# Kernel tuning notes

Measured on AMD Instinct MI355X. Metric: run time of the kernel, lower is better.

## Reference

```python
import jax, jax.numpy as jnp
import numpy as np

D_MODEL = 1024
N_HEADS = 16
HEAD_DIM = D_MODEL // N_HEADS
Q_PROJ = D_MODEL // 2
KV_PROJ = D_MODEL
INIT_SCALE = 0.02
EPS = 1e-5


def _ln(x, g, b):
    mu = jnp.mean(x, axis=-1, keepdims=True)
    var = jnp.mean(jnp.square(x - mu), axis=-1, keepdims=True)
    return (x - mu) * jax.lax.rsqrt(var + EPS) * g + b


def setup_inputs() -> dict:
    key = jax.random.key(0)
    ks = jax.random.split(key, 8)
    B, S = 2, 2048
    x = jax.random.normal(ks[0], (B, S, D_MODEL), dtype=jnp.float32)
    W_dq = INIT_SCALE * jax.random.normal(ks[1], (D_MODEL, Q_PROJ), dtype=jnp.float32)
    W_uq = INIT_SCALE * jax.random.normal(ks[2], (Q_PROJ, D_MODEL), dtype=jnp.float32)
    W_dkv = INIT_SCALE * jax.random.normal(ks[3], (D_MODEL, KV_PROJ), dtype=jnp.float32)
    W_ukv = INIT_SCALE * jax.random.normal(ks[4], (KV_PROJ, 2 * D_MODEL), dtype=jnp.float32)
    wo = INIT_SCALE * jax.random.normal(ks[5], (D_MODEL, D_MODEL), dtype=jnp.float32)
    return {
        "x": x,
        "W_dq": W_dq, "W_uq": W_uq,
        "q_ln_g": jnp.ones((Q_PROJ,), jnp.float32), "q_ln_b": jnp.zeros((Q_PROJ,), jnp.float32),
        "W_dkv": W_dkv, "W_ukv": W_ukv,
        "kv_ln_g": jnp.ones((KV_PROJ,), jnp.float32), "kv_ln_b": jnp.zeros((KV_PROJ,), jnp.float32),
        "preq_g": jnp.ones((D_MODEL,), jnp.float32), "preq_b": jnp.zeros((D_MODEL,), jnp.float32),
        "prekv_g": jnp.ones((D_MODEL,), jnp.float32), "prekv_b": jnp.zeros((D_MODEL,), jnp.float32),
        "wo": wo,
    }


def reference(x, W_dq, W_uq, q_ln_g, q_ln_b, W_dkv, W_ukv, kv_ln_g, kv_ln_b,
              preq_g, preq_b, prekv_g, prekv_b, wo):
    B, S, D = x.shape
    H, dh = N_HEADS, HEAD_DIM
    # Q path: pre-norm -> low-rank down -> LN -> up
    x_q = _ln(x, preq_g, preq_b)
    cq = _ln(x_q @ W_dq, q_ln_g, q_ln_b)            # [B,S,D/2]
    Q = (cq @ W_uq).reshape(B, S, H, dh)             # [B,S,H,dh]
    Q = Q / jnp.sqrt(jnp.asarray(dh, x.dtype))
    # KV path: pre-norm -> compress -> LN -> up, split into K,V
    x_kv = _ln(x, prekv_g, prekv_b)
    ckv = _ln(x_kv @ W_dkv, kv_ln_g, kv_ln_b)        # [B,S,D]
    KV = ckv @ W_ukv                                 # [B,S,2D]
    K, V = jnp.split(KV, 2, axis=-1)
    K = K.reshape(B, S, H, dh)
    V = V.reshape(B, S, H, dh)
    # causal attention (scores materialized as in original)
    scores = jnp.einsum('bqhd,bkhd->bhqk', Q, K)     # [B,H,S,S]
    causal = jnp.tril(jnp.ones((S, S), dtype=bool))  # True where allowed
    scores = jnp.where(causal[None, None], scores, jnp.asarray(-jnp.inf, scores.dtype))
    attn = jax.nn.softmax(scores, axis=-1)
    out = jnp.einsum('bhqk,bkhd->bqhd', attn, V).reshape(B, S, D)
    return out @ wo.T
```

## Files before the change

### kernel.cpp

```cpp
#include <hip/hip_runtime.h>
#include <hip/hip_bf16.h>

#define SEQ   2048
#define BATCH 2
#define NROWS 4096
#define DM    1024
#define NHEAD 16
#define DH    64
#define QP    512
#define KVP   1024
#define CH    4

typedef unsigned short us;
typedef ushort4 us4;
using bf16x8 = __attribute__((ext_vector_type(8))) __bf16;
using f32x4  = __attribute__((ext_vector_type(4))) float;

__device__ __forceinline__ us f2bf(float f) {
  union { __hip_bfloat16 h; us u; } cv;
  cv.h = __float2bfloat16(f);
  return cv.u;
}
__device__ __forceinline__ float bf2f(us u) {
  union { unsigned int u32; float f; } cv;
  cv.u32 = ((unsigned int)u) << 16;
  return cv.f;
}
__device__ __forceinline__ float loadp(const void* p, long i, int isbf) {
  return isbf ? bf2f(((const us*)p)[i]) : ((const float*)p)[i];
}
__device__ __forceinline__ void async16(const void* g, void* l) {
  __builtin_amdgcn_global_load_lds((__attribute__((address_space(1))) void*)g,
                                   (__attribute__((address_space(3))) void*)l,
                                   16, 0, 0);
}
__device__ __forceinline__ unsigned cvtpk(float lo, float hi) {
  unsigned r;
  asm("v_cvt_pk_bf16_f32 %0, %1, %2" : "=v"(r) : "v"(lo), "v"(hi));
  return r;
}

__global__ void detect_dtype(const us* __restrict__ xu, int* __restrict__ flag) {
  __shared__ int red[256];
  const int tid = threadIdx.x;
  int cnt = 0;
  for (int i = tid; i < 4096; i += 256) {
    const int e = (xu[i] >> 7) & 0xff;
    if (e == 0 || (e >= 100 && e <= 134)) cnt++;
  }
  red[tid] = cnt;
  __syncthreads();
  for (int s = 128; s; s >>= 1) {
    if (tid < s) red[tid] += red[tid + s];
    __syncthreads();
  }
  if (tid == 0) *flag = (red[0] >= 3900) ? 1 : 0;
}

struct TD { const void* in; us* out; int R, C, nt, trans; };

__global__ __launch_bounds__(256) void stage0(
    TD t0, TD t1, TD t2, TD t3, TD t4,
    float4* __restrict__ zp, int n4,
    const void* __restrict__ xin,
    const void* __restrict__ g1, const void* __restrict__ b1,
    const void* __restrict__ g2, const void* __restrict__ b2,
    us* __restrict__ out1, us* __restrict__ out2,
    const int* __restrict__ flag)
{
  __shared__ us tile[32][33];
  __shared__ float red[8];
  __shared__ float musd[2];
  const int tid = threadIdx.x;
  const int isbf = *flag;
  int lin = blockIdx.x;

  if (lin < 5120) {
    TD t = t0;
    if (lin >= t.nt) { lin -= t.nt; t = t1;
      if (lin >= t.nt) { lin -= t.nt; t = t2;
        if (lin >= t.nt) { lin -= t.nt; t = t3;
          if (lin >= t.nt) { lin -= t.nt; t = t4; } } } }
    const int ntx = t.C >> 5;
    const int by = lin / ntx, bx = lin - by * ntx;
    const int tx = tid & 31, ty = tid >> 5;
    const long r0 = (long)by * 32, c0 = (long)bx * 32;
    if (t.trans) {
#pragma unroll
      for (int i = 0; i < 32; i += 8)
        tile[ty + i][tx] = isbf ? ((const us*)t.in)[(r0 + ty + i) * t.C + c0 + tx]
                                : f2bf(((const float*)t.in)[(r0 + ty + i) * t.C + c0 + tx]);
      __syncthreads();
#pragma unroll
      for (int i = 0; i < 32; i += 8)
        t.out[(c0 + ty + i) * t.R + r0 + tx] = tile[tx][ty + i];
    } else {
#pragma unroll
      for (int i = 0; i < 32; i += 8)
        t.out[(r0 + ty + i) * t.C + c0 + tx] =
            isbf ? ((const us*)t.in)[(r0 + ty + i) * t.C + c0 + tx]
                 : f2bf(((const float*)t.in)[(r0 + ty + i) * t.C + c0 + tx]);
    }
    return;
  }
  if (lin < 6144) {
    const float4 z = {0.f, 0.f, 0.f, 0.f};
    for (int i = (lin - 5120) * 256 + tid; i < n4; i += 1024 * 256) zp[i] = z;
    return;
  }
  const long row = lin - 6144;
  float v[4];
  float s = 0.f, s2 = 0.f;
#pragma unroll
  for (int i = 0; i < 4; i++) {
    const long c = tid + i * 256;
    const float t = loadp(xin, row * 1024 + c, isbf);
    v[i] = t; s += t; s2 += t * t;
  }
#pragma unroll
  for (int off = 32; off > 0; off >>= 1) {
    s  += __shfl_down(s,  off);
    s2 += __shfl_down(s2, off);
  }
  const int wave = tid >> 6, lane = tid & 63;
  if (lane == 0) { red[wave] = s; red[4 + wave] = s2; }
  __syncthreads();
  if (tid == 0) {
    const float ts = red[0] + red[1] + red[2] + red[3];
    const float t2 = red[4] + red[5] + red[6] + red[7];
    const float mu = ts * (1.f / 1024.f);
    const float var = t2 * (1.f / 1024.f) - mu * mu;
    musd[0] = mu; musd[1] = rsqrtf(var + 1e-5f);
  }
  __syncthreads();
  const float mu = musd[0], rs = musd[1];
#pragma unroll
  for (int i = 0; i < 4; i++) {
    const long c = tid + i * 256;
    const float nrm = (v[i] - mu) * rs;
    out1[row * 1024 + c] = f2bf(nrm * loadp(g1, c, isbf) + loadp(b1, c, isbf));
    out2[row * 1024 + c] = f2bf(nrm * loadp(g2, c, isbf) + loadp(b2, c, isbf));
  }
}

template<int C>
__device__ __forceinline__ void ln_body(const us* __restrict__ in,
                                        const void* __restrict__ g, const void* __restrict__ b,
                                        us* __restrict__ out, long row, int tid, int isbf) {
  constexpr int NP = C / 256;
  float v[NP];
  float s = 0.f, s2 = 0.f;
#pragma unroll
  for (int i = 0; i < NP; i++) {
    const float t = bf2f(in[row * C + tid + i * 256]);
    v[i] = t; s += t; s2 += t * t;
  }
#pragma unroll
  for (int off = 32; off > 0; off >>= 1) {
    s  += __shfl_down(s,  off);
    s2 += __shfl_down(s2, off);
  }
  __shared__ float red[8];
  __shared__ float musd[2];
  const int wave = tid >> 6, lane = tid & 63;
  if (lane == 0) { red[wave] = s; red[4 + wave] = s2; }
  __syncthreads();
  if (tid == 0) {
    const float ts = red[0] + red[1] + red[2] + red[3];
    const float t2 = red[4] + red[5] + red[6] + red[7];
    const float mu = ts * (1.f / C);
    const float var = t2 * (1.f / C) - mu * mu;
    musd[0] = mu; musd[1] = rsqrtf(var + 1e-5f);
  }
  __syncthreads();
  const float mu = musd[0], rs = musd[1];
#pragma unroll
  for (int i = 0; i < NP; i++) {
    const long c = tid + i * 256;
    out[row * C + c] = f2bf((v[i] - mu) * rs * loadp(g, c, isbf) + loadp(b, c, isbf));
  }
}

__global__ __launch_bounds__(256) void ln_rows_pair(
    const us* __restrict__ inq, const void* __restrict__ qg, const void* __restrict__ qb,
    us* __restrict__ outq,
    const us* __restrict__ inkv, const void* __restrict__ kvg, const void* __restrict__ kvb,
    us* __restrict__ outkv,
    const int* __restrict__ flag)
{
  const int isbf = *flag;
  if (blockIdx.x < NROWS)
    ln_body<512>(inq, qg, qb, outq, blockIdx.x, threadIdx.x, isbf);
  else
    ln_body<1024>(inkv, kvg, kvb, outkv, blockIdx.x - NROWS, threadIdx.x, isbf);
}

struct GD { const us* A; const us* Bt; void* C; int N, K, nxs; float scale; int omode; };

__global__ __launch_bounds__(256) void gemm_mt(GD g0, GD g1, int nb0,
                                               const int* __restrict__ flag) {
  __shared__ us As[2][128 * 32];
  __shared__ us Bs[2][128 * 32];
  GD g;
  int lin = blockIdx.x;
  {
    const int cpx = gridDim.x >> 3;
    lin = (lin & 7) * cpx + (lin >> 3);
  }
  if (lin < nb0) g = g0; else { g = g1; lin -= nb0; }
  const int by = lin >> g.nxs;
  const int bx = lin - (by << g.nxs);
  const int N = g.N, K = g.K;

  const int tid  = threadIdx.x;
  const int lane = tid & 63;
  const int wave = tid >> 6;
  const int n16  = lane & 15;
  const int quad = lane >> 4;
  const long m0 = (long)by * 128;
  const long n0 = (long)bx * 128;
  const int wm = (wave >> 1) * 64;
  const int wn = (wave & 1) * 64;

  const f32x4 zero = {0.f, 0.f, 0.f, 0.f};
  f32x4 acc[4][4];
#pragma unroll
  for (int i = 0; i < 4; i++)
#pragma unroll
    for (int j = 0; j < 4; j++) acc[i][j] = zero;

  const int srow = tid >> 2;
  const int scol = (tid & 3) * 8;
  const us* Ag0 = g.A  + (m0 + srow) * K + scol;
  const us* Ag1 = g.A  + (m0 + 64 + srow) * K + scol;
  const us* Bg0 = g.Bt + (n0 + srow) * K + scol;
  const us* Bg1 = g.Bt + (n0 + 64 + srow) * K + scol;
  const int lds_off = srow * 32 + scol;

  for (int k0 = 0; k0 < K; k0 += 64) {
#pragma unroll
    for (int s = 0; s < 2; s++) {
      const int ks = k0 + s * 32;
      async16(Ag0 + ks, As[s] + lds_off);
      async16(Ag1 + ks, As[s] + 2048 + lds_off);
      async16(Bg0 + ks, Bs[s] + lds_off);
      async16(Bg1 + ks, Bs[s] + 2048 + lds_off);
    }
    __syncthreads();
#pragma unroll
    for (int s = 0; s < 2; s++) {
      bf16x8 af[4], bfv[4];
#pragma unroll
      for (int i = 0; i < 4; i++)
        af[i] = *(const bf16x8*)(As[s] + (wm + i * 16 + n16) * 32 + quad * 8);
#pragma unroll
      for (int j = 0; j < 4; j++)
        bfv[j] = *(const bf16x8*)(Bs[s] + (wn + j * 16 + n16) * 32 + quad * 8);
#pragma unroll
      for (int i = 0; i < 4; i++)
#pragma unroll
        for (int j = 0; j < 4; j++)
          acc[i][j] = __builtin_amdgcn_mfma_f32_16x16x32_bf16(af[i], bfv[j], acc[i][j], 0, 0, 0);
    }
    __syncthreads();
  }

  const bool obf = (g.omode == 1) || (g.omode == 2 && *flag != 0);
  float* Cf = (float*)g.C;
  us* Cb = (us*)g.C;
#pragma unroll
  for (int i = 0; i < 4; i++) {
    const long row = m0 + wm + i * 16 + quad * 4;
#pragma unroll
    for (int j = 0; j < 4; j++) {
      const long col = n0 + wn + j * 16 + n16;
#pragma unroll
      for (int r = 0; r < 4; r++) {
        const float v = acc[i][j][r] * g.scale;
        if (obf) Cb[(row + r) * N + col] = f2bf(v);
        else     Cf[(row + r) * N + col] = v;
      }
    }
  }
}

#define SWZ(row, col) ((row) * 64 + ((col) ^ (((row) & 7) << 3)))

__global__ __launch_bounds__(256, 4) void flash_attn(
    const us* __restrict__ Q, const us* __restrict__ KV,
    float* __restrict__ Oacc, float* __restrict__ Lacc)
{
  __shared__ us Ks[64 * 64];
  __shared__ us Vt[64 * 64];

  int lin = blockIdx.x;
  int qt = 31, nc = 0;
  for (; qt >= 0; --qt) { nc = (qt >> 2) + 1; if (lin < nc) break; lin -= nc; }
  const int chunk = lin;
  const int kt0 = chunk * CH;
  const int kt1 = min(kt0 + CH, qt + 1);

  const int h   = blockIdx.y;
  const int bb  = blockIdx.z;
  const int tid = threadIdx.x;
  const int lane = tid & 63;
  const int wave = tid >> 6;
  const int n16 = lane & 15;
  const int quad = lane >> 4;
  const int qbase = qt * 64;
  const long rowQ0 = (long)bb * SEQ;

  bf16x8 aq[2];
  {
    const long gq = (rowQ0 + qbase + wave * 16 + n16) * DM + h * DH;
    aq[0] = *(const bf16x8*)(Q + gq + quad * 8);
    aq[1] = *(const bf16x8*)(Q + gq + 32 + quad * 8);
  }

  const f32x4 zero = {0.f, 0.f, 0.f, 0.f};
  f32x4 oacc[4];
#pragma unroll
  for (int d = 0; d < 4; d++) oacc[d] = zero;
  float rsum = 0.f;

  const int kk_key = tid >> 3;
  const int kk_d8  = (tid & 7) * 8;
  const int vd  = tid & 63;
  const int vw  = tid >> 6;
  const int vkb = vw * 8;

  const us* kgb = KV + (rowQ0 + kk_key) * 2048 + h * DH + kk_d8;
  const us* vgb = KV + (rowQ0 + vw * 4) * 2048 + KVP + h * DH + vd;

  uint4 kpre0, kpre1;
  us vraw[16];
  auto loadKV = [&](int kt) {
    const us* kg = kgb + (long)kt * (64 * 2048);
    kpre0 = *(const uint4*)kg;
    kpre1 = *(const uint4*)(kg + 32 * 2048);
    const us* vg = vgb + (long)kt * (64 * 2048);
#pragma unroll
    for (int r = 0; r < 4; r++) {
      vraw[r]      = vg[r * 2048];
      vraw[4 + r]  = vg[(16 + r) * 2048];
      vraw[8 + r]  = vg[(32 + r) * 2048];
      vraw[12 + r] = vg[(48 + r) * 2048];
    }
  };
  loadKV(kt0);

  for (int kt = kt0; kt < kt1; kt++) {
    __syncthreads();
    *(uint4*)(Ks + SWZ(kk_key, kk_d8))      = kpre0;
    *(uint4*)(Ks + SWZ(kk_key + 32, kk_d8)) = kpre1;
    {
      uint4 p0, p1;
      p0.x = (unsigned)vraw[0]  | ((unsigned)vraw[1]  << 16);
      p0.y = (unsigned)vraw[2]  | ((unsigned)vraw[3]  << 16);
      p0.z = (unsigned)vraw[4]  | ((unsigned)vraw[5]  << 16);
      p0.w = (unsigned)vraw[6]  | ((unsigned)vraw[7]  << 16);
      p1.x = (unsigned)vraw[8]  | ((unsigned)vraw[9]  << 16);
      p1.y = (unsigned)vraw[10] | ((unsigned)vraw[11] << 16);
      p1.z = (unsigned)vraw[12] | ((unsigned)vraw[13] << 16);
      p1.w = (unsigned)vraw[14] | ((unsigned)vraw[15] << 16);
      *(uint4*)(Vt + SWZ(vd, vkb))      = p0;
      *(uint4*)(Vt + SWZ(vd, vkb + 32)) = p1;
    }
    __syncthreads();
    if (kt + 1 < kt1) loadKV(kt + 1);

    f32x4 sv[4];
#pragma unroll
    for (int j = 0; j < 4; j++) {
      const bf16x8 ak0 = *(const bf16x8*)(Ks + SWZ(j * 16 + n16, quad * 8));
      const bf16x8 ak1 = *(const bf16x8*)(Ks + SWZ(j * 16 + n16, 32 + quad * 8));
      f32x4 s = zero;
      s = __builtin_amdgcn_mfma_f32_16x16x32_bf16(ak0, aq[0], s, 0, 0, 0);
      s = __builtin_amdgcn_mfma_f32_16x16x32_bf16(ak1, aq[1], s, 0, 0, 0);
      sv[j] = s;
    }

    if (kt == qt) {
      const int qrl = wave * 16 + n16;
#pragma unroll
      for (int j = 0; j < 4; j++) {
        const int kl = j * 16 + quad * 4;
#pragma unroll
        for (int r = 0; r < 4; r++)
          sv[j][r] = (kl + r <= qrl) ? sv[j][r] : -1e30f;
      }
    }

    unsigned pep[4][2];
#pragma unroll
    for (int j = 0; j < 4; j++) {
      const float p0 = __builtin_amdgcn_exp2f(sv[j][0]);
      const float p1 = __builtin_amdgcn_exp2f(sv[j][1]);
      const float p2 = __builtin_amdgcn_exp2f(sv[j][2]);
      const float p3 = __builtin_amdgcn_exp2f(sv[j][3]);
      rsum += (p0 + p1) + (p2 + p3);
      pep[j][0] = cvtpk(p0, p1);
      pep[j][1] = cvtpk(p2, p3);
    }

    __builtin_amdgcn_s_setprio(1);
#pragma unroll
    for (int kc = 0; kc < 2; kc++) {
      union { bf16x8 v; unsigned u[4]; } apu;
      apu.u[0] = pep[2 * kc][0];
      apu.u[1] = pep[2 * kc][1];
      apu.u[2] = pep[2 * kc + 1][0];
      apu.u[3] = pep[2 * kc + 1][1];
#pragma unroll
      for (int d = 0; d < 4; d++) {
        const bf16x8 bv = *(const bf16x8*)(Vt + SWZ(d * 16 + n16, kc * 32 + quad * 8));
        oacc[d] = __builtin_amdgcn_mfma_f32_16x16x32_bf16(apu.v, bv, oacc[d], 0, 0, 0);
      }
    }
    __builtin_amdgcn_s_setprio(0);
  }

  rsum += __shfl_xor(rsum, 16);
  rsum += __shfl_xor(rsum, 32);

  const long rw0 = rowQ0 + qbase + wave * 16;
  if (quad == 0)
    atomicAdd(&Lacc[(rw0 + n16) * NHEAD + h], rsum);
#pragma unroll
  for (int r = 0; r < 4; r++) {
    float* dst = Oacc + (rw0 + quad * 4 + r) * DM + h * DH + n16;
#pragma unroll
    for (int d = 0; d < 4; d++)
      atomicAdd(dst + d * 16, oacc[d][r]);
  }
}

__global__ __launch_bounds__(256) void flash_combine(
    const float* __restrict__ Oacc, const float* __restrict__ Lacc,
    us* __restrict__ O)
{
  __shared__ float invl[NHEAD];
  const long row = blockIdx.x;
  const int tid = threadIdx.x;
  if (tid < NHEAD) invl[tid] = 1.f / Lacc[row * NHEAD + tid];
  __syncthreads();
#pragma unroll
  for (int i = 0; i < 4; i++) {
    const int col = tid + i * 256;
    O[row * DM + col] = f2bf(Oacc[row * DM + col] * invl[col >> 6]);
  }
}

extern "C" void kernel_launch(void* const* d_in, const int* in_sizes, int n_in,
                              void* d_out, int out_size, void* d_ws, size_t ws_size,
                              hipStream_t stream) {
  const void* x      = d_in[0];
  const void* Wdq    = d_in[1];
  const void* Wuq    = d_in[2];
  const void* qg     = d_in[3];
  const void* qb     = d_in[4];
  const void* Wdkv   = d_in[5];
  const void* Wukv   = d_in[6];
  const void* kvg    = d_in[7];
  const void* kvb    = d_in[8];
  const void* preqg  = d_in[9];
  const void* preqb  = d_in[10];
  const void* prekvg = d_in[11];
  const void* prekvb = d_in[12];
  const void* wo     = d_in[13];

  char* ws = (char*)d_ws;
  const long MB = 1 << 20;
  int* flag   = (int*)ws;
  us* wdq_t   = (us*)(ws + 1 * MB);
  us* wuq_t   = (us*)(ws + 2 * MB);
  us* wdkv_t  = (us*)(ws + 3 * MB);
  us* wukv_t  = (us*)(ws + 5 * MB);
  us* wo_c    = (us*)(ws + 9 * MB);
  us* xq      = (us*)(ws + 11 * MB);
  us* xkv     = (us*)(ws + 19 * MB);
  float* Oacc = (float*)(ws + 27 * MB);
  float* Lacc = (float*)(ws + 43 * MB);
  us* obuf    = (us*)(ws + 43 * MB + 256 * 1024);
  us* tq_bf   = obuf;
  us* cq      = (us*)(ws + 43 * MB + 256 * 1024 + 8 * MB);
  us* qbuf    = (us*)(ws + 43 * MB + 256 * 1024 + 12 * MB);
  us* tkv_bf  = qbuf;
  us* ckv     = (us*)(ws + 43 * MB + 256 * 1024 + 20 * MB);
  us* kv      = (us*)(ws + 43 * MB + 256 * 1024 + 28 * MB);

  {
    static int hflag;
    const long xb = (long)in_sizes[0];
    int known = -1;
    if (xb == (long)BATCH * SEQ * DM * 4) known = 0;
    else if (xb == (long)BATCH * SEQ * DM * 2) known = 1;
    if (known >= 0) {
      hflag = known;
      hipMemcpyAsync(flag, &hflag, sizeof(int), hipMemcpyHostToDevice, stream);
    } else {
      detect_dtype<<<1, 256, 0, stream>>>((const us*)x, flag);
    }
  }

  {
    TD t0 = { Wdq,  wdq_t,  1024,  512,  512, 1 };
    TD t1 = { Wuq,  wuq_t,   512, 1024,  512, 1 };
    TD t2 = { Wdkv, wdkv_t, 1024, 1024, 1024, 1 };
    TD t3 = { Wukv, wukv_t, 1024, 2048, 2048, 1 };
    TD t4 = { wo,   wo_c,   1024, 1024, 1024, 0 };
    const int n4 = (16 * 1024 * 1024 + 256 * 1024) / 16;
    stage0<<<10240, 256, 0, stream>>>(t0, t1, t2, t3, t4,
                                      (float4*)Oacc, n4,
                                      x, preqg, preqb, prekvg, prekvb, xq, xkv, flag);
  }

  {
    GD g0 = { xq,  wdq_t,  tq_bf,   512, 1024, 2, 1.f, 1 };
    GD g1 = { xkv, wdkv_t, tkv_bf, 1024, 1024, 3, 1.f, 1 };
    gemm_mt<<<384, 256, 0, stream>>>(g0, g1, 128, flag);
  }

  ln_rows_pair<<<2 * NROWS, 256, 0, stream>>>(tq_bf, qg, qb, cq, tkv_bf, kvg, kvb, ckv, flag);

  {
    GD g0 = { cq,  wuq_t,  qbuf, 1024,  512, 3, 0.125f * 1.44269504f, 1 };
    GD g1 = { ckv, wukv_t, kv,   2048, 1024, 4, 1.f, 1 };
    gemm_mt<<<768, 256, 0, stream>>>(g0, g1, 256, flag);
  }

  flash_attn<<<dim3(144, NHEAD, BATCH), 256, 0, stream>>>(qbuf, kv, Oacc, Lacc);
  flash_combine<<<NROWS, 256, 0, stream>>>(Oacc, Lacc, obuf);

  {
    GD g0 = { obuf, wo_c, d_out, 1024, 1024, 3, 1.f, 2 };
    gemm_mt<<<256, 256, 0, stream>>>(g0, g0, 256, flag);
  }
}
```

Before: 298.3 us.

## Replace split-K flash attention with one block per query tile

Flash attention now processes the full causal key range for each query tile in a single block and normalizes and writes bf16 output directly. This removes the fp32 atomic accumulation into Oacc/Lacc, the zero-fill of those buffers in stage0, and the separate combine kernel. The cost is far less parallelism: 1024 blocks instead of 4608, with heavy load imbalance since the longest tiles process 32 key tiles serially.

```diff
diff --git a/kernel.cpp b/kernel.cpp
--- a/kernel.cpp
+++ b/kernel.cpp
@@ -9,7 +9,6 @@
 #define DH    64
 #define QP    512
 #define KVP   1024
-#define CH    4
 
 typedef unsigned short us;
 typedef ushort4 us4;
@@ -61,7 +60,6 @@
 
 __global__ __launch_bounds__(256) void stage0(
     TD t0, TD t1, TD t2, TD t3, TD t4,
-    float4* __restrict__ zp, int n4,
     const void* __restrict__ xin,
     const void* __restrict__ g1, const void* __restrict__ b1,
     const void* __restrict__ g2, const void* __restrict__ b2,
@@ -103,12 +101,7 @@
     }
     return;
   }
-  if (lin < 6144) {
-    const float4 z = {0.f, 0.f, 0.f, 0.f};
-    for (int i = (lin - 5120) * 256 + tid; i < n4; i += 1024 * 256) zp[i] = z;
-    return;
-  }
-  const long row = lin - 6144;
+  const long row = lin - 5120;
   float v[4];
   float s = 0.f, s2 = 0.f;
 #pragma unroll
@@ -288,17 +281,13 @@
 
 __global__ __launch_bounds__(256, 4) void flash_attn(
     const us* __restrict__ Q, const us* __restrict__ KV,
-    float* __restrict__ Oacc, float* __restrict__ Lacc)
+    us* __restrict__ O)
 {
   __shared__ us Ks[64 * 64];
   __shared__ us Vt[64 * 64];
 
-  int lin = blockIdx.x;
-  int qt = 31, nc = 0;
-  for (; qt >= 0; --qt) { nc = (qt >> 2) + 1; if (lin < nc) break; lin -= nc; }
-  const int chunk = lin;
-  const int kt0 = chunk * CH;
-  const int kt1 = min(kt0 + CH, qt + 1);
+  const int qt = 31 - (int)blockIdx.x;
+  const int nt = qt + 1;
 
   const int h   = blockIdx.y;
   const int bb  = blockIdx.z;
@@ -347,9 +336,9 @@
       vraw[12 + r] = vg[(48 + r) * 2048];
     }
   };
-  loadKV(kt0);
-
-  for (int kt = kt0; kt < kt1; kt++) {
+  loadKV(0);
+
+  for (int kt = 0; kt < nt; kt++) {
     __syncthreads();
     *(uint4*)(Ks + SWZ(kk_key, kk_d8))      = kpre0;
     *(uint4*)(Ks + SWZ(kk_key + 32, kk_d8)) = kpre1;
@@ -367,7 +356,7 @@
       *(uint4*)(Vt + SWZ(vd, vkb + 32)) = p1;
     }
     __syncthreads();
-    if (kt + 1 < kt1) loadKV(kt + 1);
+    if (kt + 1 < nt) loadKV(kt + 1);
 
     f32x4 sv[4];
 #pragma unroll
@@ -422,32 +411,16 @@
 
   rsum += __shfl_xor(rsum, 16);
   rsum += __shfl_xor(rsum, 32);
+  const float inv = 1.f / rsum;
 
   const long rw0 = rowQ0 + qbase + wave * 16;
-  if (quad == 0)
-    atomicAdd(&Lacc[(rw0 + n16) * NHEAD + h], rsum);
 #pragma unroll
   for (int r = 0; r < 4; r++) {
-    float* dst = Oacc + (rw0 + quad * 4 + r) * DM + h * DH + n16;
+    const float invr = __shfl(inv, quad * 4 + r);
+    us* dst = O + (rw0 + quad * 4 + r) * DM + h * DH + n16;
 #pragma unroll
     for (int d = 0; d < 4; d++)
-      atomicAdd(dst + d * 16, oacc[d][r]);
-  }
-}
-
-__global__ __launch_bounds__(256) void flash_combine(
-    const float* __restrict__ Oacc, const float* __restrict__ Lacc,
-    us* __restrict__ O)
-{
-  __shared__ float invl[NHEAD];
-  const long row = blockIdx.x;
-  const int tid = threadIdx.x;
-  if (tid < NHEAD) invl[tid] = 1.f / Lacc[row * NHEAD + tid];
-  __syncthreads();
-#pragma unroll
-  for (int i = 0; i < 4; i++) {
-    const int col = tid + i * 256;
-    O[row * DM + col] = f2bf(Oacc[row * DM + col] * invl[col >> 6]);
+      dst[d * 16] = f2bf(oacc[d][r] * invr);
   }
 }
 
@@ -479,15 +452,13 @@
   us* wo_c    = (us*)(ws + 9 * MB);
   us* xq      = (us*)(ws + 11 * MB);
   us* xkv     = (us*)(ws + 19 * MB);
-  float* Oacc = (float*)(ws + 27 * MB);
-  float* Lacc = (float*)(ws + 43 * MB);
-  us* obuf    = (us*)(ws + 43 * MB + 256 * 1024);
+  us* obuf    = (us*)(ws + 27 * MB);
   us* tq_bf   = obuf;
-  us* cq      = (us*)(ws + 43 * MB + 256 * 1024 + 8 * MB);
-  us* qbuf    = (us*)(ws + 43 * MB + 256 * 1024 + 12 * MB);
+  us* cq      = (us*)(ws + 35 * MB);
+  us* qbuf    = (us*)(ws + 39 * MB);
   us* tkv_bf  = qbuf;
-  us* ckv     = (us*)(ws + 43 * MB + 256 * 1024 + 20 * MB);
-  us* kv      = (us*)(ws + 43 * MB + 256 * 1024 + 28 * MB);
+  us* ckv     = (us*)(ws + 47 * MB);
+  us* kv      = (us*)(ws + 55 * MB);
 
   {
     static int hflag;
@@ -509,10 +480,8 @@
     TD t2 = { Wdkv, wdkv_t, 1024, 1024, 1024, 1 };
     TD t3 = { Wukv, wukv_t, 1024, 2048, 2048, 1 };
     TD t4 = { wo,   wo_c,   1024, 1024, 1024, 0 };
-    const int n4 = (16 * 1024 * 1024 + 256 * 1024) / 16;
-    stage0<<<10240, 256, 0, stream>>>(t0, t1, t2, t3, t4,
-                                      (float4*)Oacc, n4,
-                                      x, preqg, preqb, prekvg, prekvb, xq, xkv, flag);
+    stage0<<<9216, 256, 0, stream>>>(t0, t1, t2, t3, t4,
+                                     x, preqg, preqb, prekvg, prekvb, xq, xkv, flag);
   }
 
   {
@@ -529,8 +498,7 @@
     gemm_mt<<<768, 256, 0, stream>>>(g0, g1, 256, flag);
   }
 
-  flash_attn<<<dim3(144, NHEAD, BATCH), 256, 0, stream>>>(qbuf, kv, Oacc, Lacc);
-  flash_combine<<<NROWS, 256, 0, stream>>>(Oacc, Lacc, obuf);
+  flash_attn<<<dim3(32, NHEAD, BATCH), 256, 0, stream>>>(qbuf, kv, obuf);
 
   {
     GD g0 = { obuf, wo_c, d_out, 1024, 1024, 3, 1.f, 2 };
```

After: 263.6 us. -11.6%, faster.
